# Kernel optimization log

Measured on AMD Instinct MI355X. Metric: run time of the kernel, lower is better.

The kernel has to match this reference:

```python
import jax, jax.numpy as jnp
import numpy as np

B, N, D_IN, D_OUT, H = 2, 2048, 1024, 1024, 16
HD = D_OUT // H


def setup_inputs() -> dict:
    key = jax.random.key(0)
    ks = jax.random.split(key, 6)
    s_in = 1.0 / np.sqrt(D_IN)
    s_out = 1.0 / np.sqrt(D_OUT)
    return {
        "x": jax.random.normal(ks[0], (B, N, D_IN), dtype=jnp.float32),
        "Wq": jax.random.uniform(ks[1], (D_IN, D_OUT), jnp.float32, -s_in, s_in),
        "Wk": jax.random.uniform(ks[2], (D_IN, D_OUT), jnp.float32, -s_in, s_in),
        "Wv": jax.random.uniform(ks[3], (D_IN, D_OUT), jnp.float32, -s_in, s_in),
        "Wo": jax.random.uniform(ks[4], (D_OUT, D_OUT), jnp.float32, -s_out, s_out),
        "bo": jax.random.uniform(ks[5], (D_OUT,), jnp.float32, -s_out, s_out),
    }


def reference(x, Wq, Wk, Wv, Wo, bo):
    b, n, _ = x.shape
    # project and split heads: [b, n, d_out] -> [b, h, n, hd]
    def heads(w):
        return w.reshape(b, n, H, HD).transpose(0, 2, 1, 3)
    q = heads(x @ Wq)
    k = heads(x @ Wk)
    v = heads(x @ Wv)
    # materialized causal attention (dropout rate 0.0 -> identity)
    scores = jnp.einsum("bhqd,bhkd->bhqk", q, k)
    causal = jnp.tril(jnp.ones((n, n), dtype=bool))  # keep lower triangle
    scores = jnp.where(causal, scores, -jnp.inf)
    attn = jax.nn.softmax(scores / np.sqrt(HD), axis=-1)
    ctx = jnp.einsum("bhqk,bhkd->bhqd", attn, v)
    ctx = ctx.transpose(0, 2, 1, 3).reshape(b, n, D_OUT)
    return ctx @ Wo + bo
```

## Files before the change

kernel.cpp:

```cpp
#include <hip/hip_runtime.h>
#include <math.h>
#include <stdint.h>

#define B_ 2
#define N_ 2048
#define D_ 1024
#define H_ 16
#define HD_ 64
#define M_ (B_ * N_)

typedef __bf16 bf16x8 __attribute__((ext_vector_type(8)));
typedef float f32x4 __attribute__((ext_vector_type(4)));

__device__ __forceinline__ ushort bfbits(float f) {
    __bf16 h = (__bf16)f;
    return __builtin_bit_cast(ushort, h);
}

__device__ __forceinline__ void glds16(const ushort* g, ushort* l) {
    __builtin_amdgcn_global_load_lds(
        (const __attribute__((address_space(1))) uint32_t*)g,
        (__attribute__((address_space(3))) uint32_t*)l, 16, 0, 0);
}

__global__ __launch_bounds__(256) void cvt_x(const float* __restrict__ x,
                                             ushort* __restrict__ xb) {
    int i = blockIdx.x * 256 + threadIdx.x;
    float4 v = ((const float4*)x)[i];
    ushort4 o;
    o.x = bfbits(v.x); o.y = bfbits(v.y); o.z = bfbits(v.z); o.w = bfbits(v.w);
    ((ushort4*)xb)[i] = o;
}

__global__ __launch_bounds__(256) void cvt_w(const float* __restrict__ W0,
                                             const float* __restrict__ W1,
                                             const float* __restrict__ W2,
                                             const float* __restrict__ W3,
                                             ushort* __restrict__ Wt) {
    __shared__ float T[32][33];
    const float* W = (blockIdx.z == 0) ? W0 : (blockIdx.z == 1) ? W1
                   : (blockIdx.z == 2) ? W2 : W3;
    ushort* out = Wt + (size_t)blockIdx.z * D_ * D_;
    const int t = threadIdx.x;
    const int k0 = blockIdx.x * 32, n0 = blockIdx.y * 32;
    {
        int kl = t >> 3, nl = (t & 7) * 4;
        float4 v = *(const float4*)&W[(size_t)(k0 + kl) * D_ + n0 + nl];
        T[kl][nl] = v.x; T[kl][nl + 1] = v.y; T[kl][nl + 2] = v.z; T[kl][nl + 3] = v.w;
    }
    __syncthreads();
    {
        int nl = t >> 3, k4 = (t & 7) * 4;
        ushort4 o;
        o.x = bfbits(T[k4 + 0][nl]); o.y = bfbits(T[k4 + 1][nl]);
        o.z = bfbits(T[k4 + 2][nl]); o.w = bfbits(T[k4 + 3][nl]);
        *(ushort4*)&out[(size_t)(n0 + nl) * D_ + k0 + k4] = o;
    }
}

#define BK 32

__device__ __forceinline__ void gemm_tile(const ushort* __restrict__ A,
                                          const ushort* __restrict__ Bt,
                                          int K, int tileM, int tileN,
                                          ushort* As, ushort* Bs,
                                          f32x4 acc[4][4]) {
    const int t = threadIdx.x;
    const int l = t & 63;
    const int w = __builtin_amdgcn_readfirstlane(t >> 6);
    const int wr = w >> 1, wc = w & 1;
    const int li = l & 15, lg = l >> 4;
    const int lr = l >> 2;
    const int colu = (((l & 3) ^ (lr & 3)) << 3);
    const int swz = (li & 3) << 3;

    for (int k0 = 0; k0 < K; k0 += BK) {
        __syncthreads();
        #pragma unroll
        for (int it = 0; it < 2; ++it) {
            const int c2 = it * 4 + w;
            const int row = c2 * 16 + lr;
            glds16(&A[(size_t)(tileM + row) * K + k0 + colu], &As[c2 * 512]);
            glds16(&Bt[(size_t)(tileN + row) * K + k0 + colu], &Bs[c2 * 512]);
        }
        __syncthreads();
        bf16x8 a[4], b[4];
        #pragma unroll
        for (int m = 0; m < 4; ++m)
            a[m] = *(const bf16x8*)&As[(wr * 64 + m * 16 + li) * 32 + ((lg << 3) ^ swz)];
        #pragma unroll
        for (int n = 0; n < 4; ++n)
            b[n] = *(const bf16x8*)&Bs[(wc * 64 + n * 16 + li) * 32 + ((lg << 3) ^ swz)];
        #pragma unroll
        for (int m = 0; m < 4; ++m)
            #pragma unroll
            for (int n = 0; n < 4; ++n)
                acc[m][n] = __builtin_amdgcn_mfma_f32_16x16x32_bf16(a[m], b[n], acc[m][n], 0, 0, 0);
    }
}

#define QSCALE 0.180336880f

__global__ __launch_bounds__(256) void qkv_gemm(const ushort* __restrict__ xb,
                                                const ushort* __restrict__ Wt,
                                                ushort* __restrict__ q,
                                                ushort* __restrict__ k,
                                                ushort* __restrict__ vt) {
    __shared__ ushort As[128 * 32];
    __shared__ ushort Bs[128 * 32];
    __shared__ ushort Eps[128][130];
    f32x4 acc[4][4];
    #pragma unroll
    for (int m = 0; m < 4; ++m)
        #pragma unroll
        for (int n = 0; n < 4; ++n)
            acc[m][n] = (f32x4){0.f, 0.f, 0.f, 0.f};

    const int tileM = blockIdx.x * 128;
    const int wsel = blockIdx.y >> 3;
    const int tileN = (blockIdx.y & 7) * 128;
    const ushort* Bmat = Wt + (size_t)wsel * D_ * D_;

    gemm_tile(xb, Bmat, D_, tileM, tileN, As, Bs, acc);

    const int t = threadIdx.x;
    const int l = t & 63, w = t >> 6;
    const int wr = w >> 1, wc = w & 1;
    const int li = l & 15, lg = l >> 4;
    const float scale = (wsel == 0) ? QSCALE : 1.0f;

    if (wsel < 2) {
        #pragma unroll
        for (int m = 0; m < 4; ++m)
            #pragma unroll
            for (int n = 0; n < 4; ++n)
                #pragma unroll
                for (int r = 0; r < 4; ++r)
                    Eps[wr * 64 + m * 16 + lg * 4 + r][wc * 64 + n * 16 + li] =
                        bfbits(acc[m][n][r] * scale);
    } else {
        #pragma unroll
        for (int m = 0; m < 4; ++m)
            #pragma unroll
            for (int n = 0; n < 4; ++n)
                #pragma unroll
                for (int r = 0; r < 4; ++r)
                    Eps[wc * 64 + n * 16 + li][wr * 64 + m * 16 + lg * 4 + r] =
                        bfbits(acc[m][n][r]);
    }
    __syncthreads();

    const int rr = t >> 3;
    const int cb = (t & 7) * 16;
    if (wsel < 2) {
        ushort* out = (wsel == 0) ? q : k;
        #pragma unroll
        for (int it = 0; it < 4; ++it) {
            const int row = it * 32 + rr;
            uint4 v0 = *(const uint4*)&Eps[row][cb];
            uint4 v1 = *(const uint4*)&Eps[row][cb + 8];
            size_t base = (size_t)(tileM + row) * D_ + tileN + cb;
            *(uint4*)&out[base] = v0;
            *(uint4*)&out[base + 8] = v1;
        }
    } else {
        const int b = tileM >> 11;
        const int n0 = (tileM & (N_ - 1)) + cb;
        #pragma unroll
        for (int it = 0; it < 4; ++it) {
            const int row = it * 32 + rr;
            const int gcol = tileN + row;
            const int h = gcol >> 6, hd = gcol & 63;
            uint4 v0 = *(const uint4*)&Eps[row][cb];
            uint4 v1 = *(const uint4*)&Eps[row][cb + 8];
            size_t base = ((size_t)(b * H_ + h) * HD_ + hd) * N_ + n0;
            *(uint4*)&vt[base] = v0;
            *(uint4*)&vt[base + 8] = v1;
        }
    }
}

__global__ __launch_bounds__(256) void out_gemm(const ushort* __restrict__ ctx,
                                                const ushort* __restrict__ Wt,
                                                const float* __restrict__ bo,
                                                float* __restrict__ outp) {
    __shared__ ushort As[128 * 32];
    __shared__ ushort Bs[128 * 32];
    __shared__ float Epf[32][132];
    f32x4 acc[4][4];
    #pragma unroll
    for (int m = 0; m < 4; ++m)
        #pragma unroll
        for (int n = 0; n < 4; ++n)
            acc[m][n] = (f32x4){0.f, 0.f, 0.f, 0.f};

    const int tileM = blockIdx.x * 128;
    const int tileN = blockIdx.y * 128;
    const ushort* Bmat = Wt + (size_t)3 * D_ * D_;

    gemm_tile(ctx, Bmat, D_, tileM, tileN, As, Bs, acc);

    const int t = threadIdx.x;
    const int l = t & 63, w = t >> 6;
    const int wr = w >> 1, wc = w & 1;
    const int li = l & 15, lg = l >> 4;
    const int lrow = t & 31;
    const int coff = (t >> 5) * 16;

    float bias[4];
    #pragma unroll
    for (int n = 0; n < 4; ++n) bias[n] = bo[tileN + wc * 64 + n * 16 + li];

    #pragma unroll
    for (int m = 0; m < 4; ++m) {
        __syncthreads();
        #pragma unroll
        for (int n = 0; n < 4; ++n)
            #pragma unroll
            for (int r = 0; r < 4; ++r)
                Epf[wr * 16 + lg * 4 + r][wc * 64 + n * 16 + li] = acc[m][n][r] + bias[n];
        __syncthreads();
        const int grow = tileM + (lrow >> 4) * 64 + m * 16 + (lrow & 15);
        #pragma unroll
        for (int j = 0; j < 4; ++j) {
            float4 vv = *(const float4*)&Epf[lrow][coff + j * 4];
            *(float4*)&outp[(size_t)grow * D_ + tileN + coff + j * 4] = vv;
        }
    }
}

__device__ __forceinline__ void qk_mfma(f32x4 st[4], const ushort* Kb,
                                        const bf16x8 bq[2],
                                        int li, int lg, int rswz) {
    #pragma unroll
    for (int c = 0; c < 4; ++c) {
        st[c] = (f32x4){0.f, 0.f, 0.f, 0.f};
        #pragma unroll
        for (int tk = 0; tk < 2; ++tk) {
            bf16x8 kf = *(const bf16x8*)&Kb[(c * 16 + li) * 64 + (((tk * 4 + lg) ^ rswz) * 8)];
            st[c] = __builtin_amdgcn_mfma_f32_16x16x32_bf16(kf, bq[tk], st[c], 0, 0, 0);
        }
    }
}

__device__ __forceinline__ void softmax_pv(f32x4 st[4], const ushort* Vb,
                                           bool masked, int jkb, int qg,
                                           int li, int lg, int rswz,
                                           ushort* PsW, float& lsum,
                                           f32x4 od[4]) {
    if (masked) {
        #pragma unroll
        for (int c = 0; c < 4; ++c)
            #pragma unroll
            for (int r = 0; r < 4; ++r) {
                const int kgl = jkb * 64 + c * 16 + lg * 4 + r;
                if (kgl > qg) st[c][r] = -INFINITY;
            }
    }
    float rs = 0.f;
    #pragma unroll
    for (int c = 0; c < 4; ++c) {
        float p0 = exp2f(st[c][0]);
        float p1 = exp2f(st[c][1]);
        float p2 = exp2f(st[c][2]);
        float p3 = exp2f(st[c][3]);
        rs += (p0 + p1) + (p2 + p3);
        uint32_t w0, w1;
        asm("v_cvt_pk_bf16_f32 %0, %1, %2" : "=v"(w0) : "v"(p0), "v"(p1));
        asm("v_cvt_pk_bf16_f32 %0, %1, %2" : "=v"(w1) : "v"(p2), "v"(p3));
        uint2 pk; pk.x = w0; pk.y = w1;
        *(uint2*)&PsW[li * 72 + c * 16 + lg * 4] = pk;
    }
    rs += __shfl_xor(rs, 16);
    rs += __shfl_xor(rs, 32);
    lsum += rs;
    #pragma unroll
    for (int tj = 0; tj < 2; ++tj) {
        bf16x8 pa = *(const bf16x8*)&PsW[li * 72 + tj * 32 + lg * 8];
        #pragma unroll
        for (int db = 0; db < 4; ++db) {
            bf16x8 bv = *(const bf16x8*)&Vb[(db * 16 + li) * 64 + (((tj * 4 + lg) ^ rswz) * 8)];
            od[db] = __builtin_amdgcn_mfma_f32_16x16x32_bf16(pa, bv, od[db], 0, 0, 0);
        }
    }
}

__global__ __launch_bounds__(256) void attn_fwd(const ushort* __restrict__ q,
                                                const ushort* __restrict__ k,
                                                const ushort* __restrict__ vt,
                                                ushort* __restrict__ ctx) {
    __shared__ ushort Ks[2][4096];
    __shared__ ushort Vs[3][4096];
    __shared__ ushort Ps[4][16][72];

    const int t = threadIdx.x;
    const int l = t & 63;
    const int w = __builtin_amdgcn_readfirstlane(t >> 6);
    const int li = l & 15, lg = l >> 4;
    const int f = blockIdx.x;
    const int bh = ((f & 7) << 2) | ((f >> 3) & 3);
    const int qt = 31 - (f >> 5);
    const int b = bh >> 4, h = bh & 15;

    const ushort* Qg = q + ((size_t)b * N_) * D_ + h * 64;
    const ushort* Kg = k + ((size_t)b * N_) * D_ + h * 64;
    const ushort* Vg = vt + (size_t)bh * HD_ * N_;
    ushort* PsW = &Ps[w][0][0];

    const int r8 = l >> 3;
    const int soff = ((l & 7) ^ r8) * 8;
    const int rswz = li & 7;

    const int qb64 = qt * 64 + w * 16;
    const int qg = qb64 + li;

    bf16x8 bq[2];
    #pragma unroll
    for (int tk = 0; tk < 2; ++tk)
        bq[tk] = *(const bf16x8*)&Qg[(size_t)qg * D_ + tk * 32 + lg * 8];

    f32x4 od[4];
    #pragma unroll
    for (int db = 0; db < 4; ++db) od[db] = (f32x4){0.f, 0.f, 0.f, 0.f};
    float lsum = 0.f;

    #pragma unroll
    for (int i = 0; i < 2; ++i) {
        const int seg = w + i * 4;
        const int row = seg * 8 + r8;
        glds16(&Kg[(size_t)row * D_ + soff], &Ks[0][seg * 512]);
        glds16(&Vg[(size_t)row * N_ + soff], &Vs[0][seg * 512]);
    }
    __syncthreads();

    f32x4 stp[4];
    if (qt >= 1) {
        #pragma unroll
        for (int i = 0; i < 2; ++i) {
            const int seg = w + i * 4;
            const int row = seg * 8 + r8;
            glds16(&Kg[(size_t)(64 + row) * D_ + soff], &Ks[1][seg * 512]);
            glds16(&Vg[(size_t)row * N_ + 64 + soff], &Vs[1][seg * 512]);
        }
    }
    qk_mfma(stp, Ks[0], bq, li, lg, rswz);
    __syncthreads();

    int vwr = 2;
    int vrd = 0;
    for (int i = 1; i <= qt; ++i) {
        if (i + 1 <= qt) {
            #pragma unroll
            for (int ii = 0; ii < 2; ++ii) {
                const int seg = w + ii * 4;
                const int row = seg * 8 + r8;
                glds16(&Kg[(size_t)((i + 1) * 64 + row) * D_ + soff], &Ks[(i + 1) & 1][seg * 512]);
                glds16(&Vg[(size_t)row * N_ + (i + 1) * 64 + soff], &Vs[vwr][seg * 512]);
            }
        }
        f32x4 stc[4];
        qk_mfma(stc, Ks[i & 1], bq, li, lg, rswz);
        softmax_pv(stp, Vs[vrd], false, i - 1, qg, li, lg, rswz, PsW, lsum, od);
        #pragma unroll
        for (int c = 0; c < 4; ++c) stp[c] = stc[c];
        __syncthreads();
        vwr = (vwr == 2) ? 0 : vwr + 1;
        vrd = (vrd == 2) ? 0 : vrd + 1;
    }
    softmax_pv(stp, Vs[vrd], true, qt, qg, li, lg, rswz, PsW, lsum, od);

    #pragma unroll
    for (int r = 0; r < 4; ++r) {
        const float inv = 1.f / __shfl(lsum, lg * 4 + r);
        const int grow = qb64 + lg * 4 + r;
        #pragma unroll
        for (int db = 0; db < 4; ++db)
            ctx[((size_t)(b * N_ + grow)) * D_ + h * 64 + db * 16 + li] = bfbits(od[db][r] * inv);
    }
}

extern "C" void kernel_launch(void* const* d_in, const int* in_sizes, int n_in,
                              void* d_out, int out_size, void* d_ws, size_t ws_size,
                              hipStream_t stream) {
    (void)in_sizes; (void)n_in; (void)out_size; (void)ws_size;
    const float* x  = (const float*)d_in[0];
    const float* Wq = (const float*)d_in[1];
    const float* Wk = (const float*)d_in[2];
    const float* Wv = (const float*)d_in[3];
    const float* Wo = (const float*)d_in[4];
    const float* bo = (const float*)d_in[5];
    float* outp = (float*)d_out;

    ushort* xb  = (ushort*)d_ws;
    ushort* Wt  = xb + (size_t)M_ * D_;
    ushort* qb  = Wt + (size_t)4 * D_ * D_;
    ushort* kb  = qb + (size_t)M_ * D_;
    ushort* vtb = kb + (size_t)M_ * D_;
    ushort* ctx = vtb + (size_t)M_ * D_;

    cvt_x<<<dim3((M_ * D_ / 4) / 256), 256, 0, stream>>>(x, xb);
    cvt_w<<<dim3(32, 32, 4), 256, 0, stream>>>(Wq, Wk, Wv, Wo, Wt);
    qkv_gemm<<<dim3(32, 24), 256, 0, stream>>>(xb, Wt, qb, kb, vtb);
    attn_fwd<<<dim3(1024), 256, 0, stream>>>(qb, kb, vtb, ctx);
    out_gemm<<<dim3(32, 8), 256, 0, stream>>>(ctx, Wt, bo, outp);
}
```

Measured before the change: 114.6 us.

## Simplify attention pipeline, compute row sums via MFMA, shrink LDS for occupancy

```diff
diff --git a/kernel.cpp b/kernel.cpp
--- a/kernel.cpp
+++ b/kernel.cpp
@@ -246,8 +246,8 @@
 __device__ __forceinline__ void softmax_pv(f32x4 st[4], const ushort* Vb,
                                            bool masked, int jkb, int qg,
                                            int li, int lg, int rswz,
-                                           ushort* PsW, float& lsum,
-                                           f32x4 od[4]) {
+                                           ushort* PsW, f32x4& lacc,
+                                           f32x4 od[4], bf16x8 ones) {
     if (masked) {
         #pragma unroll
         for (int c = 0; c < 4; ++c)
@@ -257,26 +257,23 @@
                 if (kgl > qg) st[c][r] = -INFINITY;
             }
     }
-    float rs = 0.f;
+    const int sw = li & 7;
     #pragma unroll
     for (int c = 0; c < 4; ++c) {
         float p0 = exp2f(st[c][0]);
         float p1 = exp2f(st[c][1]);
         float p2 = exp2f(st[c][2]);
         float p3 = exp2f(st[c][3]);
-        rs += (p0 + p1) + (p2 + p3);
         uint32_t w0, w1;
         asm("v_cvt_pk_bf16_f32 %0, %1, %2" : "=v"(w0) : "v"(p0), "v"(p1));
         asm("v_cvt_pk_bf16_f32 %0, %1, %2" : "=v"(w1) : "v"(p2), "v"(p3));
         uint2 pk; pk.x = w0; pk.y = w1;
-        *(uint2*)&PsW[li * 72 + c * 16 + lg * 4] = pk;
-    }
-    rs += __shfl_xor(rs, 16);
-    rs += __shfl_xor(rs, 32);
-    lsum += rs;
+        *(uint2*)&PsW[li * 64 + (((c * 2 + (lg >> 1)) ^ sw) << 3) + ((lg & 1) << 2)] = pk;
+    }
     #pragma unroll
     for (int tj = 0; tj < 2; ++tj) {
-        bf16x8 pa = *(const bf16x8*)&PsW[li * 72 + tj * 32 + lg * 8];
+        bf16x8 pa = *(const bf16x8*)&PsW[li * 64 + (((tj * 4 + lg) ^ sw) << 3)];
+        lacc = __builtin_amdgcn_mfma_f32_16x16x32_bf16(pa, ones, lacc, 0, 0, 0);
         #pragma unroll
         for (int db = 0; db < 4; ++db) {
             bf16x8 bv = *(const bf16x8*)&Vb[(db * 16 + li) * 64 + (((tj * 4 + lg) ^ rswz) * 8)];
@@ -285,13 +282,13 @@
     }
 }
 
-__global__ __launch_bounds__(256) void attn_fwd(const ushort* __restrict__ q,
-                                                const ushort* __restrict__ k,
-                                                const ushort* __restrict__ vt,
-                                                ushort* __restrict__ ctx) {
+__global__ __launch_bounds__(256, 4) void attn_fwd(const ushort* __restrict__ q,
+                                                   const ushort* __restrict__ k,
+                                                   const ushort* __restrict__ vt,
+                                                   ushort* __restrict__ ctx) {
     __shared__ ushort Ks[2][4096];
-    __shared__ ushort Vs[3][4096];
-    __shared__ ushort Ps[4][16][72];
+    __shared__ ushort Vs[2][4096];
+    __shared__ ushort Ps[4][1024];
 
     const int t = threadIdx.x;
     const int l = t & 63;
@@ -305,7 +302,7 @@
     const ushort* Qg = q + ((size_t)b * N_) * D_ + h * 64;
     const ushort* Kg = k + ((size_t)b * N_) * D_ + h * 64;
     const ushort* Vg = vt + (size_t)bh * HD_ * N_;
-    ushort* PsW = &Ps[w][0][0];
+    ushort* PsW = &Ps[w][0];
 
     const int r8 = l >> 3;
     const int soff = ((l & 7) ^ r8) * 8;
@@ -319,10 +316,14 @@
     for (int tk = 0; tk < 2; ++tk)
         bq[tk] = *(const bf16x8*)&Qg[(size_t)qg * D_ + tk * 32 + lg * 8];
 
+    bf16x8 ones;
+    #pragma unroll
+    for (int i = 0; i < 8; ++i) ones[i] = (__bf16)1.0f;
+
     f32x4 od[4];
     #pragma unroll
     for (int db = 0; db < 4; ++db) od[db] = (f32x4){0.f, 0.f, 0.f, 0.f};
-    float lsum = 0.f;
+    f32x4 lacc = (f32x4){0.f, 0.f, 0.f, 0.f};
 
     #pragma unroll
     for (int i = 0; i < 2; ++i) {
@@ -333,45 +334,30 @@
     }
     __syncthreads();
 
-    f32x4 stp[4];
-    if (qt >= 1) {
+    int cur = 0;
+    for (int kb = 0; kb < qt; ++kb) {
         #pragma unroll
         for (int i = 0; i < 2; ++i) {
             const int seg = w + i * 4;
             const int row = seg * 8 + r8;
-            glds16(&Kg[(size_t)(64 + row) * D_ + soff], &Ks[1][seg * 512]);
-            glds16(&Vg[(size_t)row * N_ + 64 + soff], &Vs[1][seg * 512]);
-        }
-    }
-    qk_mfma(stp, Ks[0], bq, li, lg, rswz);
-    __syncthreads();
-
-    int vwr = 2;
-    int vrd = 0;
-    for (int i = 1; i <= qt; ++i) {
-        if (i + 1 <= qt) {
-            #pragma unroll
-            for (int ii = 0; ii < 2; ++ii) {
-                const int seg = w + ii * 4;
-                const int row = seg * 8 + r8;
-                glds16(&Kg[(size_t)((i + 1) * 64 + row) * D_ + soff], &Ks[(i + 1) & 1][seg * 512]);
-                glds16(&Vg[(size_t)row * N_ + (i + 1) * 64 + soff], &Vs[vwr][seg * 512]);
-            }
-        }
-        f32x4 stc[4];
-        qk_mfma(stc, Ks[i & 1], bq, li, lg, rswz);
-        softmax_pv(stp, Vs[vrd], false, i - 1, qg, li, lg, rswz, PsW, lsum, od);
-        #pragma unroll
-        for (int c = 0; c < 4; ++c) stp[c] = stc[c];
-        __syncthreads();
-        vwr = (vwr == 2) ? 0 : vwr + 1;
-        vrd = (vrd == 2) ? 0 : vrd + 1;
-    }
-    softmax_pv(stp, Vs[vrd], true, qt, qg, li, lg, rswz, PsW, lsum, od);
+            glds16(&Kg[(size_t)((kb + 1) * 64 + row) * D_ + soff], &Ks[cur ^ 1][seg * 512]);
+            glds16(&Vg[(size_t)row * N_ + (kb + 1) * 64 + soff], &Vs[cur ^ 1][seg * 512]);
+        }
+        f32x4 st[4];
+        qk_mfma(st, Ks[cur], bq, li, lg, rswz);
+        softmax_pv(st, Vs[cur], false, kb, qg, li, lg, rswz, PsW, lacc, od, ones);
+        __syncthreads();
+        cur ^= 1;
+    }
+    {
+        f32x4 st[4];
+        qk_mfma(st, Ks[cur], bq, li, lg, rswz);
+        softmax_pv(st, Vs[cur], true, qt, qg, li, lg, rswz, PsW, lacc, od, ones);
+    }
 
     #pragma unroll
     for (int r = 0; r < 4; ++r) {
-        const float inv = 1.f / __shfl(lsum, lg * 4 + r);
+        const float inv = 1.f / lacc[r];
         const int grow = qb64 + lg * 4 + r;
         #pragma unroll
         for (int db = 0; db < 4; ++db)
```

Result: faster. 111.8 us (-2.4%).
